# Kernel optimization log

Measured on AMD Instinct MI355X. Metric: run time of the kernel, lower is better.

## Reference

```python
import jax, jax.numpy as jnp
import numpy as np


def _rodrigues(axis, theta):
    # axis [..., 3] (unit), theta [...] -> rotation matrices [..., 3, 3]
    ax, ay, az = axis[..., 0], axis[..., 1], axis[..., 2]
    z = jnp.zeros_like(ax)
    K = jnp.stack([jnp.stack([z, -az, ay], -1),
                   jnp.stack([az, z, -ax], -1),
                   jnp.stack([-ay, ax, z], -1)], -2)
    s = jnp.sin(theta)[..., None, None]
    c = jnp.cos(theta)[..., None, None]
    I = jnp.eye(3, dtype=axis.dtype)
    return I + s * K + (1.0 - c) * (K @ K)


def setup_inputs() -> dict:
    B, L, NS = 8192, 16, 8
    key = jax.random.key(0)
    k = jax.random.split(key, 7)

    def unit(v):
        return v / jnp.linalg.norm(v, axis=-1, keepdims=True)

    q = 0.5 * jax.random.normal(k[0], (B, L), dtype=jnp.float32)
    joint_axes = unit(jax.random.normal(k[1], (L, 3), dtype=jnp.float32))
    # fixed per-joint URDF transforms: small random rotation + translation
    fa = unit(jax.random.normal(k[2], (L, 3), dtype=jnp.float32))
    fth = jax.random.uniform(k[3], (L,), minval=-0.3, maxval=0.3, dtype=jnp.float32)
    fixed_rot = _rodrigues(fa, fth)
    fixed_trans = 0.15 * jax.random.normal(k[4], (L, 3), dtype=jnp.float32)
    centers = 0.05 * jax.random.normal(k[5], (L, NS, 3), dtype=jnp.float32)
    radii = 0.03 + 0.05 * jax.random.uniform(k[6], (L, NS), dtype=jnp.float32)
    link_spheres = jnp.concatenate([centers, radii[..., None]], axis=-1)
    # self-collision ignore: adjacent links (and self) are ignored, like typical URDF configs
    idx = jnp.arange(L)
    collision_mask = jnp.abs(idx[:, None] - idx[None, :]) > 1  # True = pair is checked
    return {"q": q, "fixed_rot": fixed_rot, "fixed_trans": fixed_trans,
            "joint_axes": joint_axes, "link_spheres": link_spheres,
            "collision_mask": collision_mask}


def reference(q, fixed_rot, fixed_trans, joint_axes, link_spheres, collision_mask):
    B, L = q.shape
    NS = link_spheres.shape[1]

    # ---- forward kinematics: serial tree walk (parent -> child), one revolute joint per link
    def step(carry, inp):
        Rp, tp = carry                      # parent world pose [B,3,3],[B,3]
        frot, ftrans, axis, qi = inp        # [3,3],[3],[3],[B]
        Rj = _rodrigues(jnp.broadcast_to(axis, (B, 3)), qi)          # [B,3,3]
        R = jnp.einsum('bij,jk,bkl->bil', Rp, frot, Rj)
        t = tp + jnp.einsum('bij,j->bi', Rp, ftrans)
        return (R, t), (R, t)

    R0 = jnp.broadcast_to(jnp.eye(3, dtype=q.dtype), (B, 3, 3))
    t0 = jnp.zeros((B, 3), dtype=q.dtype)
    _, (Rs, ts) = jax.lax.scan(step, (R0, t0), (fixed_rot, fixed_trans, joint_axes, q.T))
    # Rs [L,B,3,3], ts [L,B,3]

    # ---- transform collision spheres to world frame: [B,L,NS,3]
    centers_w = jnp.einsum('lbij,lsj->blsi', Rs, link_spheres[..., :3]) \
        + ts.transpose(1, 0, 2)[:, :, None, :]

    # ---- pairwise sphere penetration distance (r_i + r_j - ||c_i - c_j||)
    N = L * NS
    cn = centers_w.reshape(B, N, 3)
    sq = jnp.sum(cn * cn, axis=-1)                                   # [B,N]
    d2 = sq[:, :, None] + sq[:, None, :] - 2.0 * jnp.einsum('bnd,bmd->bnm', cn, cn)
    dist = jnp.sqrt(jnp.maximum(d2, 1e-12))                          # [B,N,N]
    r = link_spheres[..., 3].reshape(N)
    pen = r[None, :, None] + r[None, None, :] - dist                 # [B,N,N]

    # per link-pair max over sphere pairs -> [B,L,L]
    pair = jnp.max(pen.reshape(B, L, NS, L, NS), axis=(2, 4))
    # ignored pairs / diagonal get -100 (matches dist buffer init in find_link_distance)
    pair = jnp.where(collision_mask[None, :, :], pair, jnp.float32(-100.0))
    link_dist = jnp.max(pair, axis=-1)                               # [B,L]
    return link_dist
```

## Files before the change

### kernel.cpp

```cpp
#include <hip/hip_runtime.h>

typedef float v2f __attribute__((ext_vector_type(2)));

#define SCHED_FENCE() __builtin_amdgcn_sched_barrier(0)

template<int CTRL>
__device__ __forceinline__ float dppmov(float x) {
    return __builtin_bit_cast(float,
        __builtin_amdgcn_update_dpp(0, __builtin_bit_cast(int, x),
                                    CTRL, 0xf, 0xf, true));
}
#define DPP_XOR1  0xB1
#define DPP_XOR2  0x4E
#define DPP_XOR8  0x128
#define DPP_SHR(d) (0x110 | (d))

__device__ __forceinline__ void pen2j(const float4& r,
                                      v2f px, v2f py, v2f pz, v2f pw,
                                      float& mi, float& mj1, float& mj2)
{
    v2f dx = px - r.x;
    v2f dy = py - r.y;
    v2f dz = pz - r.z;
    v2f d2 = dx * dx;
    d2 = __builtin_elementwise_fma(dy, dy, d2);
    d2 = __builtin_elementwise_fma(dz, dz, d2);
    v2f pen = (pw + r.w) - (v2f){__builtin_amdgcn_sqrtf(d2.x),
                                 __builtin_amdgcn_sqrtf(d2.y)};
    mi  = fmaxf(fmaxf(mi, pen.x), pen.y);
    mj1 = fmaxf(mj1, pen.x);
    mj2 = fmaxf(mj2, pen.y);
}

__device__ __forceinline__ void pen1h(const float4& r,
                                      v2f px, v2f py, v2f pz, v2f pw,
                                      float& mi, float& mj)
{
    float dx = px.y - r.x, dy = py.y - r.y, dz = pz.y - r.z;
    float d2 = fmaf(dx, dx, fmaf(dy, dy, dz * dz));
    float p  = pw.y + r.w - __builtin_amdgcn_sqrtf(d2);
    mi = fmaxf(mi, p);
    mj = fmaxf(mj, p);
}

__global__ __launch_bounds__(256, 8) void fused_kernel(
    const float* __restrict__ q,
    const float* __restrict__ frot,
    const float* __restrict__ ftrans,
    const float* __restrict__ axes,
    const float* __restrict__ spheres,
    float* __restrict__ out,
    int B)
{
    __shared__ float4 sph[4][16 * 9];
    const int t    = threadIdx.x;
    const int w    = t >> 6;
    const int lane = t & 63;
    int b = blockIdx.x * 4 + w;
    const bool alive = (b < B);
    if (!alive) b = B - 1;

    const int l = lane & 15;
    const int g = lane >> 4;

    const float qv = q[(size_t)b * 16 + l];
    const float s = __sinf(qv), c = __cosf(qv), oc = 1.0f - c;
    const float ax = axes[3*l+0], ay = axes[3*l+1], az = axes[3*l+2];

    float R00,R01,R02,R10,R11,R12,R20,R21,R22;
    #define BUILD_ROW(Ra, Rb, Rc, base)                                         \
    {                                                                           \
        float f0 = frot[base+0], f1 = frot[base+1], f2 = frot[base+2];          \
        float u0 = fmaf(f1,az, -f2*ay);                                         \
        float u1 = fmaf(f2,ax, -f0*az);                                         \
        float u2 = fmaf(f0,ay, -f1*ax);                                         \
        float v0 = fmaf(u1,az, -u2*ay);                                         \
        float v1 = fmaf(u2,ax, -u0*az);                                         \
        float v2 = fmaf(u0,ay, -u1*ax);                                         \
        Ra = fmaf(oc,v0, fmaf(s,u0, f0));                                       \
        Rb = fmaf(oc,v1, fmaf(s,u1, f1));                                       \
        Rc = fmaf(oc,v2, fmaf(s,u2, f2));                                       \
    }
    BUILD_ROW(R00,R01,R02, 9*l+0)
    BUILD_ROW(R10,R11,R12, 9*l+3)
    BUILD_ROW(R20,R21,R22, 9*l+6)
    #undef BUILD_ROW
    float t0 = ftrans[3*l+0], t1 = ftrans[3*l+1], t2 = ftrans[3*l+2];
    SCHED_FENCE();

    #define SCAN_STEP(D, CTRL)                                                  \
    {                                                                           \
        float P00 = dppmov<CTRL>(R00), P01 = dppmov<CTRL>(R01), P02 = dppmov<CTRL>(R02); \
        float P10 = dppmov<CTRL>(R10), P11 = dppmov<CTRL>(R11), P12 = dppmov<CTRL>(R12); \
        float P20 = dppmov<CTRL>(R20), P21 = dppmov<CTRL>(R21), P22 = dppmov<CTRL>(R22); \
        float pt0 = dppmov<CTRL>(t0),  pt1 = dppmov<CTRL>(t1),  pt2 = dppmov<CTRL>(t2);  \
        const bool lo = (l < (D));                                              \
        P00 = lo ? 1.0f : P00;                                                  \
        P11 = lo ? 1.0f : P11;                                                  \
        P22 = lo ? 1.0f : P22;                                                  \
        {                                                                       \
            float n00 = fmaf(P00,R00, fmaf(P01,R10, P02*R20));                  \
            float n01 = fmaf(P00,R01, fmaf(P01,R11, P02*R21));                  \
            float n02 = fmaf(P00,R02, fmaf(P01,R12, P02*R22));                  \
            float n10 = fmaf(P10,R00, fmaf(P11,R10, P12*R20));                  \
            float n11 = fmaf(P10,R01, fmaf(P11,R11, P12*R21));                  \
            float n12 = fmaf(P10,R02, fmaf(P11,R12, P12*R22));                  \
            float n20 = fmaf(P20,R00, fmaf(P21,R10, P22*R20));                  \
            float n21 = fmaf(P20,R01, fmaf(P21,R11, P22*R21));                  \
            float n22 = fmaf(P20,R02, fmaf(P21,R12, P22*R22));                  \
            float nt0 = fmaf(P00,t0, fmaf(P01,t1, fmaf(P02,t2, pt0)));          \
            float nt1 = fmaf(P10,t0, fmaf(P11,t1, fmaf(P12,t2, pt1)));          \
            float nt2 = fmaf(P20,t0, fmaf(P21,t1, fmaf(P22,t2, pt2)));          \
            R00=n00; R01=n01; R02=n02;                                          \
            R10=n10; R11=n11; R12=n12;                                          \
            R20=n20; R21=n21; R22=n22;                                          \
            t0=nt0; t1=nt1; t2=nt2;                                             \
        }                                                                       \
    }
    SCAN_STEP(1, DPP_SHR(1))
    SCAN_STEP(2, DPP_SHR(2))
    SCAN_STEP(4, DPP_SHR(4))
    SCAN_STEP(8, DPP_SHR(8))
    #undef SCAN_STEP
    SCHED_FENCE();

    #pragma unroll
    for (int k = 0; k < 2; ++k) {
        const int sp = g * 2 + k;
        float4 cs = reinterpret_cast<const float4*>(spheres)[l*8 + sp];
        float wx = fmaf(R00,cs.x, fmaf(R01,cs.y, fmaf(R02,cs.z, t0)));
        float wy = fmaf(R10,cs.x, fmaf(R11,cs.y, fmaf(R12,cs.z, t1)));
        float wz = fmaf(R20,cs.x, fmaf(R21,cs.y, fmaf(R22,cs.z, t2)));
        sph[w][l*9 + sp] = make_float4(wx, wy, wz, cs.w);
    }
    asm volatile("s_waitcnt lgkmcnt(0)" ::: "memory");
    SCHED_FENCE();

    const float4* S  = sph[w];
    const float*  Sf = reinterpret_cast<const float*>(S);
    const int sr = lane >> 3;
    const int sc = lane & 7;
    const float4* Srow = S + sr;
    const float*  Scol = Sf + sc*4;

    float m0=-100.f,m1=-100.f,m2=-100.f,m3=-100.f,m4=-100.f,m5=-100.f,
          m6=-100.f,m7=-100.f,m8=-100.f,m9=-100.f,m10=-100.f,m11=-100.f,
          m12=-100.f,m13=-100.f,m14=-100.f,m15=-100.f;

    v2f Ax,Ay,Az,Aw, Bx,By,Bz,Bw;

    #define FILLP(Px,Py,Pz,Pw, j)                                               \
    {                                                                           \
        Px = (v2f){Scol[(j)*36+0], Scol[(j)*36+36]};                            \
        Py = (v2f){Scol[(j)*36+1], Scol[(j)*36+37]};                            \
        Pz = (v2f){Scol[(j)*36+2], Scol[(j)*36+38]};                            \
        Pw = (v2f){Scol[(j)*36+3], Scol[(j)*36+39]};                            \
    }

    FILLP(Ax,Ay,Az,Aw, 2)
    FILLP(Bx,By,Bz,Bw, 4)
    { float4 r = Srow[0*9]; pen2j(r,Ax,Ay,Az,Aw, m0,m2,m3); pen2j(r,Bx,By,Bz,Bw, m0,m4,m5); }
    { float4 r = Srow[1*9]; pen1h(r,Ax,Ay,Az,Aw, m1,m3);    pen2j(r,Bx,By,Bz,Bw, m1,m4,m5); }
    { float4 r = Srow[2*9]; pen2j(r,Bx,By,Bz,Bw, m2,m4,m5); }
    { float4 r = Srow[3*9]; pen1h(r,Bx,By,Bz,Bw, m3,m5); }
    SCHED_FENCE();

    FILLP(Ax,Ay,Az,Aw, 6)
    FILLP(Bx,By,Bz,Bw, 8)
    { float4 r = Srow[0*9]; pen2j(r,Ax,Ay,Az,Aw, m0,m6,m7); pen2j(r,Bx,By,Bz,Bw, m0,m8,m9); }
    { float4 r = Srow[1*9]; pen2j(r,Ax,Ay,Az,Aw, m1,m6,m7); pen2j(r,Bx,By,Bz,Bw, m1,m8,m9); }
    { float4 r = Srow[2*9]; pen2j(r,Ax,Ay,Az,Aw, m2,m6,m7); pen2j(r,Bx,By,Bz,Bw, m2,m8,m9); }
    { float4 r = Srow[3*9]; pen2j(r,Ax,Ay,Az,Aw, m3,m6,m7); pen2j(r,Bx,By,Bz,Bw, m3,m8,m9); }
    { float4 r = Srow[4*9]; pen2j(r,Ax,Ay,Az,Aw, m4,m6,m7); pen2j(r,Bx,By,Bz,Bw, m4,m8,m9); }
    { float4 r = Srow[5*9]; pen1h(r,Ax,Ay,Az,Aw, m5,m7);    pen2j(r,Bx,By,Bz,Bw, m5,m8,m9); }
    { float4 r = Srow[6*9]; pen2j(r,Bx,By,Bz,Bw, m6,m8,m9); }
    { float4 r = Srow[7*9]; pen1h(r,Bx,By,Bz,Bw, m7,m9); }
    SCHED_FENCE();

    FILLP(Ax,Ay,Az,Aw, 10)
    FILLP(Bx,By,Bz,Bw, 12)
    { float4 r = Srow[0*9];  pen2j(r,Ax,Ay,Az,Aw, m0,m10,m11); pen2j(r,Bx,By,Bz,Bw, m0,m12,m13); }
    { float4 r = Srow[1*9];  pen2j(r,Ax,Ay,Az,Aw, m1,m10,m11); pen2j(r,Bx,By,Bz,Bw, m1,m12,m13); }
    { float4 r = Srow[2*9];  pen2j(r,Ax,Ay,Az,Aw, m2,m10,m11); pen2j(r,Bx,By,Bz,Bw, m2,m12,m13); }
    { float4 r = Srow[3*9];  pen2j(r,Ax,Ay,Az,Aw, m3,m10,m11); pen2j(r,Bx,By,Bz,Bw, m3,m12,m13); }
    { float4 r = Srow[4*9];  pen2j(r,Ax,Ay,Az,Aw, m4,m10,m11); pen2j(r,Bx,By,Bz,Bw, m4,m12,m13); }
    { float4 r = Srow[5*9];  pen2j(r,Ax,Ay,Az,Aw, m5,m10,m11); pen2j(r,Bx,By,Bz,Bw, m5,m12,m13); }
    { float4 r = Srow[6*9];  pen2j(r,Ax,Ay,Az,Aw, m6,m10,m11); pen2j(r,Bx,By,Bz,Bw, m6,m12,m13); }
    { float4 r = Srow[7*9];  pen2j(r,Ax,Ay,Az,Aw, m7,m10,m11); pen2j(r,Bx,By,Bz,Bw, m7,m12,m13); }
    { float4 r = Srow[8*9];  pen2j(r,Ax,Ay,Az,Aw, m8,m10,m11); pen2j(r,Bx,By,Bz,Bw, m8,m12,m13); }
    { float4 r = Srow[9*9];  pen1h(r,Ax,Ay,Az,Aw, m9,m11);     pen2j(r,Bx,By,Bz,Bw, m9,m12,m13); }
    { float4 r = Srow[10*9]; pen2j(r,Bx,By,Bz,Bw, m10,m12,m13); }
    { float4 r = Srow[11*9]; pen1h(r,Bx,By,Bz,Bw, m11,m13); }
    SCHED_FENCE();

    FILLP(Ax,Ay,Az,Aw, 14)
    { float4 r = Srow[0*9];  pen2j(r,Ax,Ay,Az,Aw, m0,m14,m15); }
    { float4 r = Srow[1*9];  pen2j(r,Ax,Ay,Az,Aw, m1,m14,m15); }
    { float4 r = Srow[2*9];  pen2j(r,Ax,Ay,Az,Aw, m2,m14,m15); }
    { float4 r = Srow[3*9];  pen2j(r,Ax,Ay,Az,Aw, m3,m14,m15); }
    { float4 r = Srow[4*9];  pen2j(r,Ax,Ay,Az,Aw, m4,m14,m15); }
    { float4 r = Srow[5*9];  pen2j(r,Ax,Ay,Az,Aw, m5,m14,m15); }
    { float4 r = Srow[6*9];  pen2j(r,Ax,Ay,Az,Aw, m6,m14,m15); }
    { float4 r = Srow[7*9];  pen2j(r,Ax,Ay,Az,Aw, m7,m14,m15); }
    { float4 r = Srow[8*9];  pen2j(r,Ax,Ay,Az,Aw, m8,m14,m15); }
    { float4 r = Srow[9*9];  pen2j(r,Ax,Ay,Az,Aw, m9,m14,m15); }
    { float4 r = Srow[10*9]; pen2j(r,Ax,Ay,Az,Aw, m10,m14,m15); }
    { float4 r = Srow[11*9]; pen2j(r,Ax,Ay,Az,Aw, m11,m14,m15); }
    { float4 r = Srow[12*9]; pen2j(r,Ax,Ay,Az,Aw, m12,m14,m15); }
    { float4 r = Srow[13*9]; pen1h(r,Ax,Ay,Az,Aw, m13,m15); }
    #undef FILLP
    SCHED_FENCE();

    {
        const int bit0 = lane & 1;
        #define F1(A,C) { float s_ = bit0 ? A : C; float r_ = dppmov<DPP_XOR1>(s_); A = fmaxf(bit0 ? C : A, r_); }
        F1(m0,m8) F1(m1,m9) F1(m2,m10) F1(m3,m11) F1(m4,m12) F1(m5,m13) F1(m6,m14) F1(m7,m15)
        #undef F1
        const int bit1 = (lane >> 1) & 1;
        #define F2(A,C) { float s_ = bit1 ? A : C; float r_ = dppmov<DPP_XOR2>(s_); A = fmaxf(bit1 ? C : A, r_); }
        F2(m0,m4) F2(m1,m5) F2(m2,m6) F2(m3,m7)
        #undef F2
        const int bit2 = (lane >> 2) & 1;
        #define F4(A,C) { float s_ = bit2 ? A : C; float r_ = __shfl_xor(s_, 4, 64); A = fmaxf(bit2 ? C : A, r_); }
        F4(m0,m2) F4(m1,m3)
        #undef F4
        const int bit3 = (lane >> 3) & 1;
        { float s_ = bit3 ? m0 : m1; float r_ = dppmov<DPP_XOR8>(s_); m0 = fmaxf(bit3 ? m1 : m0, r_); }
        m0 = fmaxf(m0, __shfl_xor(m0, 16, 64));
        m0 = fmaxf(m0, __shfl_xor(m0, 32, 64));
    }

    if (alive && lane < 16) {
        int k = ((lane & 1) << 3) | ((lane & 2) << 1) | ((lane & 4) >> 1) | ((lane & 8) >> 3);
        out[(size_t)b * 16 + k] = m0;
    }
}

extern "C" void kernel_launch(void* const* d_in, const int* in_sizes, int n_in,
                              void* d_out, int out_size, void* d_ws, size_t ws_size,
                              hipStream_t stream) {
    const float* q      = (const float*)d_in[0];
    const float* frot   = (const float*)d_in[1];
    const float* ftrans = (const float*)d_in[2];
    const float* axes   = (const float*)d_in[3];
    const float* sphere = (const float*)d_in[4];
    float* out = (float*)d_out;

    const int B = in_sizes[0] / 16;
    const int blocks = (B + 3) / 4;
    fused_kernel<<<dim3(blocks), dim3(256), 0, stream>>>(
        q, frot, ftrans, axes, sphere, out, B);
}
```

Baseline: 23.69 us.

## Split fused kernel into forward-kinematics kernel and pairwise-collision kernel via workspace

```diff
diff --git a/kernel.cpp b/kernel.cpp
--- a/kernel.cpp
+++ b/kernel.cpp
@@ -15,78 +15,67 @@
 #define DPP_XOR8  0x128
 #define DPP_SHR(d) (0x110 | (d))
 
-__device__ __forceinline__ void pen2j(const float4& r,
-                                      v2f px, v2f py, v2f pz, v2f pw,
-                                      float& mi, float& mj1, float& mj2)
-{
-    v2f dx = px - r.x;
-    v2f dy = py - r.y;
-    v2f dz = pz - r.z;
-    v2f d2 = dx * dx;
-    d2 = __builtin_elementwise_fma(dy, dy, d2);
-    d2 = __builtin_elementwise_fma(dz, dz, d2);
-    v2f pen = (pw + r.w) - (v2f){__builtin_amdgcn_sqrtf(d2.x),
-                                 __builtin_amdgcn_sqrtf(d2.y)};
-    mi  = fmaxf(fmaxf(mi, pen.x), pen.y);
-    mj1 = fmaxf(mj1, pen.x);
-    mj2 = fmaxf(mj2, pen.y);
-}
-
-__device__ __forceinline__ void pen1h(const float4& r,
-                                      v2f px, v2f py, v2f pz, v2f pw,
-                                      float& mi, float& mj)
-{
-    float dx = px.y - r.x, dy = py.y - r.y, dz = pz.y - r.z;
-    float d2 = fmaf(dx, dx, fmaf(dy, dy, dz * dz));
-    float p  = pw.y + r.w - __builtin_amdgcn_sqrtf(d2);
-    mi = fmaxf(mi, p);
-    mj = fmaxf(mj, p);
-}
-
-__global__ __launch_bounds__(256, 8) void fused_kernel(
+__global__ __launch_bounds__(256, 4) void fk_kernel(
     const float* __restrict__ q,
     const float* __restrict__ frot,
     const float* __restrict__ ftrans,
     const float* __restrict__ axes,
     const float* __restrict__ spheres,
-    float* __restrict__ out,
+    float4* __restrict__ ws,
     int B)
 {
-    __shared__ float4 sph[4][16 * 9];
     const int t    = threadIdx.x;
     const int w    = t >> 6;
     const int lane = t & 63;
-    int b = blockIdx.x * 4 + w;
+    const int h    = lane >> 5;
+    int b = blockIdx.x * 8 + w * 2 + h;
     const bool alive = (b < B);
     if (!alive) b = B - 1;
 
     const int l = lane & 15;
-    const int g = lane >> 4;
+    const int g = (lane >> 4) & 1;
 
     const float qv = q[(size_t)b * 16 + l];
     const float s = __sinf(qv), c = __cosf(qv), oc = 1.0f - c;
     const float ax = axes[3*l+0], ay = axes[3*l+1], az = axes[3*l+2];
 
+    const float F00=frot[9*l+0], F01=frot[9*l+1], F02=frot[9*l+2];
+    const float F10=frot[9*l+3], F11=frot[9*l+4], F12=frot[9*l+5];
+    const float F20=frot[9*l+6], F21=frot[9*l+7], F22=frot[9*l+8];
+
     float R00,R01,R02,R10,R11,R12,R20,R21,R22;
-    #define BUILD_ROW(Ra, Rb, Rc, base)                                         \
-    {                                                                           \
-        float f0 = frot[base+0], f1 = frot[base+1], f2 = frot[base+2];          \
-        float u0 = fmaf(f1,az, -f2*ay);                                         \
-        float u1 = fmaf(f2,ax, -f0*az);                                         \
-        float u2 = fmaf(f0,ay, -f1*ax);                                         \
-        float v0 = fmaf(u1,az, -u2*ay);                                         \
-        float v1 = fmaf(u2,ax, -u0*az);                                         \
-        float v2 = fmaf(u0,ay, -u1*ax);                                         \
-        Ra = fmaf(oc,v0, fmaf(s,u0, f0));                                       \
-        Rb = fmaf(oc,v1, fmaf(s,u1, f1));                                       \
-        Rc = fmaf(oc,v2, fmaf(s,u2, f2));                                       \
-    }
-    BUILD_ROW(R00,R01,R02, 9*l+0)
-    BUILD_ROW(R10,R11,R12, 9*l+3)
-    BUILD_ROW(R20,R21,R22, 9*l+6)
-    #undef BUILD_ROW
+    {
+        float u0 = fmaf(F01,az, -F02*ay);
+        float u1 = fmaf(F02,ax, -F00*az);
+        float u2 = fmaf(F00,ay, -F01*ax);
+        float v0 = fmaf(u1,az, -u2*ay);
+        float v1 = fmaf(u2,ax, -u0*az);
+        float v2 = fmaf(u0,ay, -u1*ax);
+        R00 = fmaf(oc,v0, fmaf(s,u0, F00));
+        R01 = fmaf(oc,v1, fmaf(s,u1, F01));
+        R02 = fmaf(oc,v2, fmaf(s,u2, F02));
+
+        u0 = fmaf(F11,az, -F12*ay);
+        u1 = fmaf(F12,ax, -F10*az);
+        u2 = fmaf(F10,ay, -F11*ax);
+        v0 = fmaf(u1,az, -u2*ay);
+        v1 = fmaf(u2,ax, -u0*az);
+        v2 = fmaf(u0,ay, -u1*ax);
+        R10 = fmaf(oc,v0, fmaf(s,u0, F10));
+        R11 = fmaf(oc,v1, fmaf(s,u1, F11));
+        R12 = fmaf(oc,v2, fmaf(s,u2, F12));
+
+        u0 = fmaf(F21,az, -F22*ay);
+        u1 = fmaf(F22,ax, -F20*az);
+        u2 = fmaf(F20,ay, -F21*ax);
+        v0 = fmaf(u1,az, -u2*ay);
+        v1 = fmaf(u2,ax, -u0*az);
+        v2 = fmaf(u0,ay, -u1*ax);
+        R20 = fmaf(oc,v0, fmaf(s,u0, F20));
+        R21 = fmaf(oc,v1, fmaf(s,u1, F21));
+        R22 = fmaf(oc,v2, fmaf(s,u2, F22));
+    }
     float t0 = ftrans[3*l+0], t1 = ftrans[3*l+1], t2 = ftrans[3*l+2];
-    SCHED_FENCE();
 
     #define SCAN_STEP(D, CTRL)                                                  \
     {                                                                           \
@@ -122,16 +111,66 @@
     SCAN_STEP(4, DPP_SHR(4))
     SCAN_STEP(8, DPP_SHR(8))
     #undef SCAN_STEP
-    SCHED_FENCE();
-
+
+    float4* wsb = ws + (size_t)b * 128;
     #pragma unroll
-    for (int k = 0; k < 2; ++k) {
-        const int sp = g * 2 + k;
+    for (int k = 0; k < 4; ++k) {
+        const int sp = g * 4 + k;
         float4 cs = reinterpret_cast<const float4*>(spheres)[l*8 + sp];
         float wx = fmaf(R00,cs.x, fmaf(R01,cs.y, fmaf(R02,cs.z, t0)));
         float wy = fmaf(R10,cs.x, fmaf(R11,cs.y, fmaf(R12,cs.z, t1)));
         float wz = fmaf(R20,cs.x, fmaf(R21,cs.y, fmaf(R22,cs.z, t2)));
-        sph[w][l*9 + sp] = make_float4(wx, wy, wz, cs.w);
+        if (alive) wsb[l*8 + sp] = make_float4(wx, wy, wz, cs.w);
+    }
+}
+
+__device__ __forceinline__ void pen2j(const float4& r,
+                                      v2f px, v2f py, v2f pz, v2f pw,
+                                      float& mi, float& mj1, float& mj2)
+{
+    v2f dx = px - r.x;
+    v2f dy = py - r.y;
+    v2f dz = pz - r.z;
+    v2f d2 = dx * dx;
+    d2 = __builtin_elementwise_fma(dy, dy, d2);
+    d2 = __builtin_elementwise_fma(dz, dz, d2);
+    v2f pen = (pw + r.w) - (v2f){__builtin_amdgcn_sqrtf(d2.x),
+                                 __builtin_amdgcn_sqrtf(d2.y)};
+    mi  = fmaxf(fmaxf(mi, pen.x), pen.y);
+    mj1 = fmaxf(mj1, pen.x);
+    mj2 = fmaxf(mj2, pen.y);
+}
+
+__device__ __forceinline__ void pen1h(const float4& r,
+                                      v2f px, v2f py, v2f pz, v2f pw,
+                                      float& mi, float& mj)
+{
+    float dx = px.y - r.x, dy = py.y - r.y, dz = pz.y - r.z;
+    float d2 = fmaf(dx, dx, fmaf(dy, dy, dz * dz));
+    float p  = pw.y + r.w - __builtin_amdgcn_sqrtf(d2);
+    mi = fmaxf(mi, p);
+    mj = fmaxf(mj, p);
+}
+
+__global__ __launch_bounds__(256, 8) void pair_kernel(
+    const float4* __restrict__ ws,
+    float* __restrict__ out,
+    int B)
+{
+    __shared__ float4 sph[4][16 * 9];
+    const int t    = threadIdx.x;
+    const int w    = t >> 6;
+    const int lane = t & 63;
+    int b = blockIdx.x * 4 + w;
+    const bool alive = (b < B);
+    if (!alive) b = B - 1;
+
+    {
+        const float4* src = ws + (size_t)b * 128;
+        float4 v0 = src[lane];
+        float4 v1 = src[lane + 64];
+        sph[w][(lane >> 3) * 9 + (lane & 7)]        = v0;
+        sph[w][((lane + 64) >> 3) * 9 + (lane & 7)] = v1;
     }
     asm volatile("s_waitcnt lgkmcnt(0)" ::: "memory");
     SCHED_FENCE();
@@ -247,7 +286,8 @@
     float* out = (float*)d_out;
 
     const int B = in_sizes[0] / 16;
-    const int blocks = (B + 3) / 4;
-    fused_kernel<<<dim3(blocks), dim3(256), 0, stream>>>(
-        q, frot, ftrans, axes, sphere, out, B);
-}
+    fk_kernel<<<dim3((B + 7) / 8), dim3(256), 0, stream>>>(
+        q, frot, ftrans, axes, sphere, (float4*)d_ws, B);
+    pair_kernel<<<dim3((B + 3) / 4), dim3(256), 0, stream>>>(
+        (const float4*)d_ws, out, B);
+}
```

Measured after the change: 34.21 us. 1.44x slower.
